# Kernel tuning notes

Hardware: AMD Instinct MI355X
Metric: run time of the kernel (lower is better)

## Reference

```python
import jax, jax.numpy as jnp
import numpy as np

D_MODEL = 1024
NUM_HEADS = 16
D_K = D_MODEL // NUM_HEADS  # 64
THETA = 10000.0


def apply_rope(x, positions, theta):
    # x: [b, h, s, d_k]; interleaved-pair RoPE
    d = x.shape[-1]
    inv_freq = theta ** (-jnp.arange(0, d, 2, dtype=jnp.float32) / d)  # [d/2]
    angles = positions.astype(jnp.float32)[:, None] * inv_freq[None, :]  # [s, d/2]
    cos = jnp.cos(angles)
    sin = jnp.sin(angles)
    x1 = x[..., 0::2]
    x2 = x[..., 1::2]
    out_even = x1 * cos - x2 * sin
    out_odd = x1 * sin + x2 * cos
    return jnp.stack([out_even, out_odd], axis=-1).reshape(x.shape)


def setup_inputs() -> dict:
    key = jax.random.key(0)
    kx, kq, kk, kv, ko = jax.random.split(key, 5)
    scale = 1.0 / np.sqrt(D_MODEL)
    return {
        "x": jax.random.normal(kx, (1, 4096, D_MODEL), dtype=jnp.float32),
        "Wq": jax.random.normal(kq, (D_MODEL, D_MODEL), dtype=jnp.float32) * scale,
        "Wk": jax.random.normal(kk, (D_MODEL, D_MODEL), dtype=jnp.float32) * scale,
        "Wv": jax.random.normal(kv, (D_MODEL, D_MODEL), dtype=jnp.float32) * scale,
        "Wo": jax.random.normal(ko, (D_MODEL, D_MODEL), dtype=jnp.float32) * scale,
    }


def reference(x, Wq, Wk, Wv, Wo):
    b, s, _ = x.shape
    # Linear (no bias, weight stored as [out, in]): y = x @ W^T
    q = jnp.einsum("bsd,ed->bse", x, Wq).reshape(b, s, NUM_HEADS, D_K).transpose(0, 2, 1, 3)
    k = jnp.einsum("bsd,ed->bse", x, Wk).reshape(b, s, NUM_HEADS, D_K).transpose(0, 2, 1, 3)
    v = jnp.einsum("bsd,ed->bse", x, Wv).reshape(b, s, NUM_HEADS, D_K).transpose(0, 2, 1, 3)

    positions = jnp.arange(s)
    q = apply_rope(q, positions, THETA)
    k = apply_rope(k, positions, THETA)

    scores = jnp.einsum("bhqd,bhkd->bhqk", q, k) / jnp.sqrt(jnp.float32(D_K))
    causal = jnp.tril(jnp.ones((s, s), dtype=bool))
    scores = jnp.where(causal, scores, -jnp.inf)
    probs = jax.nn.softmax(scores, axis=-1)
    ctx = jnp.einsum("bhqk,bhkd->bhqd", probs, v)  # [b,h,s,d_k]
    ctx = ctx.transpose(0, 2, 1, 3).reshape(b, s, D_MODEL)
    return jnp.einsum("bse,de->bsd", ctx, Wo)
```

## Files before the change

### kernel.cpp

```cpp
#include <hip/hip_runtime.h>
#include <hip/hip_bf16.h>
#include <math.h>


#define S_LEN 4096
#define DMODEL 1024
#define NHEAD 16
#define QSCALE 0.1803368801111244f

typedef __attribute__((ext_vector_type(8))) short short8;
typedef __attribute__((ext_vector_type(4))) short short4_t;
typedef __attribute__((ext_vector_type(4))) float floatx4;

static __device__ __forceinline__ void load_lds16(const void* g, void* l) {
    __builtin_amdgcn_global_load_lds((const __attribute__((address_space(1))) void*)g,
                                     (__attribute__((address_space(3))) void*)l, 16, 0, 0);
}

__global__ void cvt_all_kernel(const float* __restrict__ x,  const float* __restrict__ wq,
                               const float* __restrict__ wk, const float* __restrict__ wv,
                               const float* __restrict__ wo,
                               __hip_bfloat16* __restrict__ xb,  __hip_bfloat16* __restrict__ wqb,
                               __hip_bfloat16* __restrict__ wkb, __hip_bfloat16* __restrict__ wvb,
                               __hip_bfloat16* __restrict__ wob)
{
    const size_t NX = (size_t)S_LEN * DMODEL;
    const size_t NW = (size_t)DMODEL * DMODEL;
    size_t t = ((size_t)blockIdx.x * blockDim.x + threadIdx.x) * 4;
    const float* src; __hip_bfloat16* dst; size_t off;
    if (t < NX) { src = x; dst = xb; off = t; }
    else {
        size_t j = t - NX; int seg = (int)(j >> 20); off = j & (NW - 1);
        src = (seg == 0) ? wq : (seg == 1) ? wk : (seg == 2) ? wv : wo;
        dst = (seg == 0) ? wqb : (seg == 1) ? wkb : (seg == 2) ? wvb : wob;
    }
    float4 v = *(const float4*)(src + off);
    dst[off + 0] = __float2bfloat16(v.x);
    dst[off + 1] = __float2bfloat16(v.y);
    dst[off + 2] = __float2bfloat16(v.z);
    dst[off + 3] = __float2bfloat16(v.w);
}

__global__ __launch_bounds__(256) void qkv_gemm(
    const __hip_bfloat16* __restrict__ A,
    const __hip_bfloat16* __restrict__ Bq,
    const __hip_bfloat16* __restrict__ Bk,
    const __hip_bfloat16* __restrict__ Bv,
    __hip_bfloat16* __restrict__ Qb,
    __hip_bfloat16* __restrict__ Kb,
    __hip_bfloat16* __restrict__ Vtb)
{
    __shared__ __hip_bfloat16 As[128 * 32];
    __shared__ __hip_bfloat16 Bs[128 * 32];
    const int tid  = threadIdx.x;
    const int wave = tid >> 6;
    const int lane = tid & 63;
    const int quad = lane >> 4;
    const int l15  = lane & 15;
    const int sec  = blockIdx.x >> 3;
    const __hip_bfloat16* B = (sec == 0) ? Bq : (sec == 1) ? Bk : Bv;
    const int n0 = (blockIdx.x & 7) * 128;
    const int m0 = blockIdx.y * 128;
    const int wm = (wave & 1) * 64;
    const int wn = (wave >> 1) * 64;

    floatx4 acc[4][4] = {};

    for (int kt = 0; kt < DMODEL; kt += 32) {
        #pragma unroll
        for (int p = 0; p < 2; ++p) {
            int base = (p * 4 + wave) * 1024;
            int b    = base + lane * 16;
            int row  = b >> 6;
            int ke   = (b & 63) >> 1;
            load_lds16(A + (size_t)(m0 + row) * DMODEL + kt + ke, (char*)As + base);
            load_lds16(B + (size_t)(n0 + row) * DMODEL + kt + ke, (char*)Bs + base);
        }
        __syncthreads();
        short8 af[4], bf[4];
        #pragma unroll
        for (int i = 0; i < 4; ++i)
            af[i] = *(const short8*)(As + (wm + i * 16 + l15) * 32 + quad * 8);
        #pragma unroll
        for (int j = 0; j < 4; ++j)
            bf[j] = *(const short8*)(Bs + (wn + j * 16 + l15) * 32 + quad * 8);
        #pragma unroll
        for (int i = 0; i < 4; ++i)
            #pragma unroll
            for (int j = 0; j < 4; ++j)
                acc[i][j] = __builtin_amdgcn_mfma_f32_16x16x32_bf16(af[i], bf[j], acc[i][j], 0, 0, 0);
        __syncthreads();
    }

    float ifreq[4];
    #pragma unroll
    for (int j = 0; j < 4; ++j) {
        int d = (j * 16 + l15) & 63;
        ifreq[j] = expf(-(float)(d & ~1) * (9.210340371976184f / 64.0f));
    }
    const float scale = (sec == 0) ? QSCALE : 1.0f;
    __hip_bfloat16* dst = (sec == 0) ? Qb : Kb;
    #pragma unroll
    for (int i = 0; i < 4; ++i) {
        int rowb = m0 + wm + i * 16 + quad * 4;
        #pragma unroll
        for (int j = 0; j < 4; ++j) {
            int col = n0 + wn + j * 16 + l15;
            if (sec == 2) {
                union { short4_t v; __hip_bfloat16 b[4]; } pk;
                #pragma unroll
                for (int r = 0; r < 4; ++r) pk.b[r] = __float2bfloat16(acc[i][j][r]);
                int sw = (rowb & ~63) | ((((rowb >> 3) ^ col) & 7) << 3) | (rowb & 7);
                *(short4_t*)(Vtb + (size_t)col * S_LEN + sw) = pk.v;
            } else {
                #pragma unroll
                for (int r = 0; r < 4; ++r) {
                    int rr  = rowb + r;
                    float v = acc[i][j][r];
                    float ang = (float)rr * ifreq[j];
                    float sn, cs;
                    __sincosf(ang, &sn, &cs);
                    float pv  = __shfl_xor(v, 1);
                    float out = ((lane & 1) ? (pv * sn + v * cs)
                                            : (v * cs - pv * sn)) * scale;
                    int pc = (sec == 1) ? ((col & ~63) | ((((col >> 3) ^ rr) & 7) << 3) | (col & 7))
                                        : col;
                    dst[(size_t)rr * DMODEL + pc] = __float2bfloat16(out);
                }
            }
        }
    }
}

__global__ __launch_bounds__(256) void attn_kernel(
    const __hip_bfloat16* __restrict__ Q,
    const __hip_bfloat16* __restrict__ Kb,
    const __hip_bfloat16* __restrict__ Vt,
    __hip_bfloat16* __restrict__ CTX)
{
    __shared__ __hip_bfloat16 Ks[64 * 64];
    __shared__ __hip_bfloat16 Vs[64 * 64];
    __shared__ __hip_bfloat16 Ps[4][16 * 68];
    const int b  = blockIdx.x;
    const int h  = b & 15;
    const int g  = b >> 4;
    const int gq = g >> 4, d4 = g & 15;
    const int qt = (gq == 0) ? 63 - d4 : (gq == 1) ? 32 + d4 : (gq == 2) ? 31 - d4 : d4;
    const int s0 = qt * 64;
    const int tid  = threadIdx.x;
    const int wave = tid >> 6, lane = tid & 63;
    const int quad = lane >> 4, l15 = lane & 15;
    const int k7   = l15 & 7;
    const int W    = s0 + wave * 16;

    short8 aq[2];
    {
        const __hip_bfloat16* qp = Q + (size_t)(W + l15) * DMODEL + h * 64 + quad * 8;
        aq[0] = *(const short8*)qp;
        aq[1] = *(const short8*)(qp + 32);
    }
    floatx4 o[4] = {};
    float lp[4] = {};

    for (int kt = 0; kt <= qt; ++kt) {
        #pragma unroll
        for (int p = 0; p < 4; ++p) {
            int id   = p * 4 + wave;
            int cb   = (id & 7) * 1024;
            int bb   = cb + lane * 16;
            int row  = bb >> 7;
            int ce   = (bb & 127) >> 1;
            if (id < 8)
                load_lds16(Kb + (size_t)(kt * 64 + row) * DMODEL + h * 64 + ce, (char*)Ks + cb);
            else
                load_lds16(Vt + (size_t)(h * 64 + row) * S_LEN + kt * 64 + ce,  (char*)Vs + cb);
        }
        __syncthreads();

        const int kv0 = kt * 64;
        floatx4 sc[4];
        #pragma unroll
        for (int ni = 0; ni < 4; ++ni) {
            short8 bk0 = *(const short8*)(Ks + (ni * 16 + l15) * 64 + ((quad ^ k7) << 3));
            short8 bk1 = *(const short8*)(Ks + (ni * 16 + l15) * 64 + (((4 + quad) ^ k7) << 3));
            floatx4 s = {};
            s = __builtin_amdgcn_mfma_f32_16x16x32_bf16(aq[0], bk0, s, 0, 0, 0);
            sc[ni] = __builtin_amdgcn_mfma_f32_16x16x32_bf16(aq[1], bk1, s, 0, 0, 0);
        }

        const bool edge  = (kt == qt);
        const int  rbase = W + quad * 4;
        #pragma unroll
        for (int ni = 0; ni < 4; ++ni) {
            int col = kv0 + ni * 16 + l15;
            #pragma unroll
            for (int r = 0; r < 4; ++r) {
                float p = __builtin_amdgcn_exp2f(sc[ni][r]);
                if (edge && col > rbase + r) p = 0.0f;
                lp[r] += p;
                Ps[wave][(quad * 4 + r) * 68 + ni * 16 + l15] = __float2bfloat16(p);
            }
        }

        short8 ap[2];
        #pragma unroll
        for (int dc = 0; dc < 2; ++dc) {
            const __hip_bfloat16* pp = &Ps[wave][l15 * 68 + dc * 32 + quad * 8];
            short4_t p0 = *(const short4_t*)pp;
            short4_t p1 = *(const short4_t*)(pp + 4);
            short8 a;
            a[0] = p0[0]; a[1] = p0[1]; a[2] = p0[2]; a[3] = p0[3];
            a[4] = p1[0]; a[5] = p1[1]; a[6] = p1[2]; a[7] = p1[3];
            ap[dc] = a;
        }

        #pragma unroll
        for (int od = 0; od < 4; ++od) {
            short8 bv0 = *(const short8*)(Vs + (od * 16 + l15) * 64 + ((quad ^ k7) << 3));
            short8 bv1 = *(const short8*)(Vs + (od * 16 + l15) * 64 + (((4 + quad) ^ k7) << 3));
            o[od] = __builtin_amdgcn_mfma_f32_16x16x32_bf16(ap[0], bv0, o[od], 0, 0, 0);
            o[od] = __builtin_amdgcn_mfma_f32_16x16x32_bf16(ap[1], bv1, o[od], 0, 0, 0);
        }
        __syncthreads();
    }

    #pragma unroll
    for (int r = 0; r < 4; ++r) {
        float v = lp[r];
        v += __shfl_xor(v, 1);
        v += __shfl_xor(v, 2);
        v += __shfl_xor(v, 4);
        v += __shfl_xor(v, 8);
        lp[r] = __frcp_rn(v);
    }
    #pragma unroll
    for (int od = 0; od < 4; ++od)
        #pragma unroll
        for (int r = 0; r < 4; ++r)
            CTX[(size_t)(W + quad * 4 + r) * DMODEL + h * 64 + od * 16 + l15] =
                __float2bfloat16(o[od][r] * lp[r]);
}

__global__ __launch_bounds__(256) void out_gemm(
    const __hip_bfloat16* __restrict__ A,
    const __hip_bfloat16* __restrict__ B,
    float* __restrict__ C)
{
    __shared__ __hip_bfloat16 As[128 * 32];
    __shared__ __hip_bfloat16 Bs[64 * 32];
    const int tid  = threadIdx.x;
    const int wave = tid >> 6;
    const int lane = tid & 63;
    const int quad = lane >> 4;
    const int l15  = lane & 15;
    const int n0 = blockIdx.x * 64;
    const int m0 = blockIdx.y * 128;
    const int wm = (wave & 1) * 64;
    const int wn = (wave >> 1) * 32;

    floatx4 acc[4][2] = {};

    for (int kt = 0; kt < DMODEL; kt += 32) {
        #pragma unroll
        for (int p = 0; p < 3; ++p) {
            int id  = p * 4 + wave;
            if (id < 8) {
                int base = id * 1024;
                int b    = base + lane * 16;
                int row  = b >> 6;
                int ke   = (b & 63) >> 1;
                load_lds16(A + (size_t)(m0 + row) * DMODEL + kt + ke, (char*)As + base);
            } else {
                int base = (id - 8) * 1024;
                int b    = base + lane * 16;
                int row  = b >> 6;
                int ke   = (b & 63) >> 1;
                load_lds16(B + (size_t)(n0 + row) * DMODEL + kt + ke, (char*)Bs + base);
            }
        }
        __syncthreads();
        short8 af[4], bf[2];
        #pragma unroll
        for (int i = 0; i < 4; ++i)
            af[i] = *(const short8*)(As + (wm + i * 16 + l15) * 32 + quad * 8);
        #pragma unroll
        for (int j = 0; j < 2; ++j)
            bf[j] = *(const short8*)(Bs + (wn + j * 16 + l15) * 32 + quad * 8);
        #pragma unroll
        for (int i = 0; i < 4; ++i)
            #pragma unroll
            for (int j = 0; j < 2; ++j)
                acc[i][j] = __builtin_amdgcn_mfma_f32_16x16x32_bf16(af[i], bf[j], acc[i][j], 0, 0, 0);
        __syncthreads();
    }

    #pragma unroll
    for (int i = 0; i < 4; ++i) {
        int rowb = m0 + wm + i * 16 + quad * 4;
        #pragma unroll
        for (int j = 0; j < 2; ++j) {
            int col = n0 + wn + j * 16 + l15;
            #pragma unroll
            for (int r = 0; r < 4; ++r)
                C[(size_t)(rowb + r) * DMODEL + col] = acc[i][j][r];
        }
    }
}

extern "C" void kernel_launch(void* const* d_in, const int* in_sizes, int n_in,
                              void* d_out, int out_size, void* d_ws, size_t ws_size,
                              hipStream_t stream)
{
    const float* x  = (const float*)d_in[0];
    const float* Wq = (const float*)d_in[1];
    const float* Wk = (const float*)d_in[2];
    const float* Wv = (const float*)d_in[3];
    const float* Wo = (const float*)d_in[4];

    char* ws = (char*)d_ws;
    const size_t MB = 1024 * 1024;
    __hip_bfloat16* xb  = (__hip_bfloat16*)(ws);
    __hip_bfloat16* wqb = (__hip_bfloat16*)(ws +  8 * MB);
    __hip_bfloat16* wkb = (__hip_bfloat16*)(ws + 10 * MB);
    __hip_bfloat16* wvb = (__hip_bfloat16*)(ws + 12 * MB);
    __hip_bfloat16* wob = (__hip_bfloat16*)(ws + 14 * MB);
    __hip_bfloat16* Qb  = (__hip_bfloat16*)(ws + 16 * MB);
    __hip_bfloat16* Kbf = (__hip_bfloat16*)(ws + 24 * MB);
    __hip_bfloat16* Vtb = (__hip_bfloat16*)(ws + 32 * MB);
    __hip_bfloat16* Cx  = (__hip_bfloat16*)(ws + 40 * MB);

    cvt_all_kernel<<<8192, 256, 0, stream>>>(x, Wq, Wk, Wv, Wo, xb, wqb, wkb, wvb, wob);

    qkv_gemm<<<dim3(24, 32), 256, 0, stream>>>(xb, wqb, wkb, wvb, Qb, Kbf, Vtb);

    attn_kernel<<<1024, 256, 0, stream>>>(Qb, Kbf, Vtb, Cx);

    out_gemm<<<dim3(16, 32), 256, 0, stream>>>(Cx, wob, (float*)d_out);
}
```

Baseline: 215.8 us.

## Split KV tiles across waves with fragment-packed Q/K/V layout and direct global loads

The QKV projection now writes Q, K and V in a per-head, MFMA-fragment-ordered layout. This lets the attention kernel load operand fragments straight from global memory into registers instead of staging K/V through LDS. Each wave now handles all 64 query rows of the block and a strided subset of KV tiles (split-K across waves), and the partial outputs and row sums are combined through LDS at the end. This removes per-tile __syncthreads and LDS staging. In exchange, register pressure rises with 64 accumulators per lane, and the partial outputs are rounded to bf16 before the reduction. Since no running max is kept, the exponentials are not rescaled and rely on the prescaled scores staying small.

```diff
diff --git a/kernel.cpp b/kernel.cpp
--- a/kernel.cpp
+++ b/kernel.cpp
@@ -106,13 +106,17 @@
         #pragma unroll
         for (int j = 0; j < 4; ++j) {
             int col = n0 + wn + j * 16 + l15;
+            int h   = col >> 6;
+            int hd  = col & 63;
             if (sec == 2) {
                 union { short4_t v; __hip_bfloat16 b[4]; } pk;
                 #pragma unroll
                 for (int r = 0; r < 4; ++r) pk.b[r] = __float2bfloat16(acc[i][j][r]);
-                int sw = (rowb & ~63) | ((((rowb >> 3) ^ col) & 7) << 3) | (rowb & 7);
-                *(short4_t*)(Vtb + (size_t)col * S_LEN + sw) = pk.v;
+                int od = hd >> 4, lv = hd & 15;
+                *(short4_t*)(Vtb + (size_t)h * 262144 +
+                             (((od * 512 + (rowb >> 3)) * 16 + lv) << 3) + (rowb & 7)) = pk.v;
             } else {
+                int g = hd >> 3, jj = hd & 7;
                 #pragma unroll
                 for (int r = 0; r < 4; ++r) {
                     int rr  = rowb + r;
@@ -123,89 +127,63 @@
                     float pv  = __shfl_xor(v, 1);
                     float out = ((lane & 1) ? (pv * sn + v * cs)
                                             : (v * cs - pv * sn)) * scale;
-                    int pc = (sec == 1) ? ((col & ~63) | ((((col >> 3) ^ rr) & 7) << 3) | (col & 7))
-                                        : col;
-                    dst[(size_t)rr * DMODEL + pc] = __float2bfloat16(out);
+                    dst[(size_t)h * 262144 +
+                        ((((rr >> 4) * 8 + g) * 16 + (rr & 15)) << 3) + jj] = __float2bfloat16(out);
                 }
             }
         }
     }
 }
 
-__global__ __launch_bounds__(256) void attn_kernel(
-    const __hip_bfloat16* __restrict__ Q,
-    const __hip_bfloat16* __restrict__ Kb,
-    const __hip_bfloat16* __restrict__ Vt,
-    __hip_bfloat16* __restrict__ CTX)
-{
-    __shared__ __hip_bfloat16 Ks[64 * 64];
-    __shared__ __hip_bfloat16 Vs[64 * 64];
-    __shared__ __hip_bfloat16 Ps[4][16 * 68];
-    const int b  = blockIdx.x;
-    const int h  = b & 15;
-    const int g  = b >> 4;
-    const int gq = g >> 4, d4 = g & 15;
-    const int qt = (gq == 0) ? 63 - d4 : (gq == 1) ? 32 + d4 : (gq == 2) ? 31 - d4 : d4;
-    const int s0 = qt * 64;
-    const int tid  = threadIdx.x;
-    const int wave = tid >> 6, lane = tid & 63;
-    const int quad = lane >> 4, l15 = lane & 15;
-    const int k7   = l15 & 7;
-    const int W    = s0 + wave * 16;
-
-    short8 aq[2];
-    {
-        const __hip_bfloat16* qp = Q + (size_t)(W + l15) * DMODEL + h * 64 + quad * 8;
-        aq[0] = *(const short8*)qp;
-        aq[1] = *(const short8*)(qp + 32);
-    }
-    floatx4 o[4] = {};
-    float lp[4] = {};
-
-    for (int kt = 0; kt <= qt; ++kt) {
-        #pragma unroll
-        for (int p = 0; p < 4; ++p) {
-            int id   = p * 4 + wave;
-            int cb   = (id & 7) * 1024;
-            int bb   = cb + lane * 16;
-            int row  = bb >> 7;
-            int ce   = (bb & 127) >> 1;
-            if (id < 8)
-                load_lds16(Kb + (size_t)(kt * 64 + row) * DMODEL + h * 64 + ce, (char*)Ks + cb);
-            else
-                load_lds16(Vt + (size_t)(h * 64 + row) * S_LEN + kt * 64 + ce,  (char*)Vs + cb);
-        }
-        __syncthreads();
-
-        const int kv0 = kt * 64;
-        floatx4 sc[4];
+template<bool EDGE>
+static __device__ __forceinline__ void attn_tile(
+    int kt, int quad, int l15,
+    const __hip_bfloat16* __restrict__ Kh, const __hip_bfloat16* __restrict__ Vh,
+    const short8 aq[4][2], floatx4 o[4][4], float lp[4][4],
+    __hip_bfloat16* __restrict__ PsW)
+{
+    asm volatile("s_waitcnt lgkmcnt(0)" ::: "memory");
+
+    short8 kf[4][2], vf[4][2];
+    #pragma unroll
+    for (int ni = 0; ni < 4; ++ni)
+        #pragma unroll
+        for (int dc = 0; dc < 2; ++dc)
+            kf[ni][dc] = *(const short8*)(Kh + (size_t)(((((kt*4 + ni)*8 + dc*4 + quad)*16 + l15) << 3)));
+    #pragma unroll
+    for (int od = 0; od < 4; ++od)
+        #pragma unroll
+        for (int dc = 0; dc < 2; ++dc)
+            vf[od][dc] = *(const short8*)(Vh + (size_t)((((od*512 + kt*8 + dc*4 + quad)*16 + l15) << 3)));
+
+    #pragma unroll
+    for (int g = 0; g < 4; ++g) {
+        floatx4 st[4];
         #pragma unroll
         for (int ni = 0; ni < 4; ++ni) {
-            short8 bk0 = *(const short8*)(Ks + (ni * 16 + l15) * 64 + ((quad ^ k7) << 3));
-            short8 bk1 = *(const short8*)(Ks + (ni * 16 + l15) * 64 + (((4 + quad) ^ k7) << 3));
-            floatx4 s = {};
-            s = __builtin_amdgcn_mfma_f32_16x16x32_bf16(aq[0], bk0, s, 0, 0, 0);
-            sc[ni] = __builtin_amdgcn_mfma_f32_16x16x32_bf16(aq[1], bk1, s, 0, 0, 0);
-        }
-
-        const bool edge  = (kt == qt);
-        const int  rbase = W + quad * 4;
+            floatx4 z = {};
+            floatx4 s = __builtin_amdgcn_mfma_f32_16x16x32_bf16(aq[g][0], kf[ni][0], z, 0, 0, 0);
+            st[ni]    = __builtin_amdgcn_mfma_f32_16x16x32_bf16(aq[g][1], kf[ni][1], s, 0, 0, 0);
+        }
         #pragma unroll
         for (int ni = 0; ni < 4; ++ni) {
-            int col = kv0 + ni * 16 + l15;
             #pragma unroll
             for (int r = 0; r < 4; ++r) {
-                float p = __builtin_amdgcn_exp2f(sc[ni][r]);
-                if (edge && col > rbase + r) p = 0.0f;
-                lp[r] += p;
-                Ps[wave][(quad * 4 + r) * 68 + ni * 16 + l15] = __float2bfloat16(p);
+                float e = __builtin_amdgcn_exp2f(st[ni][r]);
+                if (EDGE) {
+                    if (ni * 16 + l15 > g * 16 + quad * 4 + r) e = 0.0f;
+                }
+                lp[g][r] += e;
+                PsW[(g * 16 + quad * 4 + r) * 68 + ni * 16 + l15] = __float2bfloat16(e);
             }
         }
-
+    }
+    #pragma unroll
+    for (int g = 0; g < 4; ++g) {
         short8 ap[2];
         #pragma unroll
         for (int dc = 0; dc < 2; ++dc) {
-            const __hip_bfloat16* pp = &Ps[wave][l15 * 68 + dc * 32 + quad * 8];
+            const __hip_bfloat16* pp = PsW + (g * 16 + l15) * 68 + dc * 32 + quad * 8;
             short4_t p0 = *(const short4_t*)pp;
             short4_t p1 = *(const short4_t*)(pp + 4);
             short8 a;
@@ -213,32 +191,93 @@
             a[4] = p1[0]; a[5] = p1[1]; a[6] = p1[2]; a[7] = p1[3];
             ap[dc] = a;
         }
-
         #pragma unroll
         for (int od = 0; od < 4; ++od) {
-            short8 bv0 = *(const short8*)(Vs + (od * 16 + l15) * 64 + ((quad ^ k7) << 3));
-            short8 bv1 = *(const short8*)(Vs + (od * 16 + l15) * 64 + (((4 + quad) ^ k7) << 3));
-            o[od] = __builtin_amdgcn_mfma_f32_16x16x32_bf16(ap[0], bv0, o[od], 0, 0, 0);
-            o[od] = __builtin_amdgcn_mfma_f32_16x16x32_bf16(ap[1], bv1, o[od], 0, 0, 0);
-        }
-        __syncthreads();
-    }
+            o[g][od] = __builtin_amdgcn_mfma_f32_16x16x32_bf16(ap[0], vf[od][0], o[g][od], 0, 0, 0);
+            o[g][od] = __builtin_amdgcn_mfma_f32_16x16x32_bf16(ap[1], vf[od][1], o[g][od], 0, 0, 0);
+        }
+    }
+}
+
+__global__ __launch_bounds__(256) void attn_kernel(
+    const __hip_bfloat16* __restrict__ Q,
+    const __hip_bfloat16* __restrict__ Kp,
+    const __hip_bfloat16* __restrict__ Vp,
+    __hip_bfloat16* __restrict__ CTX)
+{
+    __shared__ __hip_bfloat16 Buf[4][64 * 68];
+    __shared__ float LPw[4][64];
+    const int b  = blockIdx.x;
+    const int h  = b & 15;
+    const int u  = 63 - (b >> 4);
+    const int tid  = threadIdx.x;
+    const int wave = tid >> 6, lane = tid & 63;
+    const int quad = lane >> 4, l15 = lane & 15;
+
+    const __hip_bfloat16* Qh = Q  + (size_t)h * 262144;
+    const __hip_bfloat16* Kh = Kp + (size_t)h * 262144;
+    const __hip_bfloat16* Vh = Vp + (size_t)h * 262144;
+    __hip_bfloat16* PsW = &Buf[wave][0];
+
+    short8 aq[4][2];
+    #pragma unroll
+    for (int g = 0; g < 4; ++g)
+        #pragma unroll
+        for (int dc = 0; dc < 2; ++dc)
+            aq[g][dc] = *(const short8*)(Qh + (size_t)(((((u*4 + g)*8 + dc*4 + quad)*16 + l15) << 3)));
+
+    floatx4 o[4][4] = {};
+    float lp[4][4] = {};
+
+    for (int kt = wave; kt < u; kt += 4)
+        attn_tile<false>(kt, quad, l15, Kh, Vh, aq, o, lp, PsW);
+    if ((u & 3) == wave)
+        attn_tile<true>(u, quad, l15, Kh, Vh, aq, o, lp, PsW);
+
+    #pragma unroll
+    for (int g = 0; g < 4; ++g)
+        #pragma unroll
+        for (int r = 0; r < 4; ++r) {
+            float v = lp[g][r];
+            v += __shfl_xor(v, 1);
+            v += __shfl_xor(v, 2);
+            v += __shfl_xor(v, 4);
+            v += __shfl_xor(v, 8);
+            lp[g][r] = v;
+        }
+    asm volatile("s_waitcnt lgkmcnt(0)" ::: "memory");
+    if (l15 == 0) {
+        #pragma unroll
+        for (int g = 0; g < 4; ++g)
+            #pragma unroll
+            for (int r = 0; r < 4; ++r)
+                LPw[wave][g * 16 + quad * 4 + r] = lp[g][r];
+    }
+    #pragma unroll
+    for (int g = 0; g < 4; ++g)
+        #pragma unroll
+        for (int od = 0; od < 4; ++od)
+            #pragma unroll
+            for (int r = 0; r < 4; ++r)
+                Buf[wave][(g * 16 + quad * 4 + r) * 68 + od * 16 + l15] =
+                    __float2bfloat16(o[g][od][r]);
+    __syncthreads();
 
     #pragma unroll
     for (int r = 0; r < 4; ++r) {
-        float v = lp[r];
-        v += __shfl_xor(v, 1);
-        v += __shfl_xor(v, 2);
-        v += __shfl_xor(v, 4);
-        v += __shfl_xor(v, 8);
-        lp[r] = __frcp_rn(v);
-    }
-    #pragma unroll
-    for (int od = 0; od < 4; ++od)
-        #pragma unroll
-        for (int r = 0; r < 4; ++r)
-            CTX[(size_t)(W + quad * 4 + r) * DMODEL + h * 64 + od * 16 + l15] =
-                __float2bfloat16(o[od][r] * lp[r]);
+        int q = wave * 16 + quad * 4 + r;
+        float ls = LPw[0][q] + LPw[1][q] + LPw[2][q] + LPw[3][q];
+        float rl = __frcp_rn(ls);
+        #pragma unroll
+        for (int od = 0; od < 4; ++od) {
+            float s = 0.0f;
+            #pragma unroll
+            for (int sl = 0; sl < 4; ++sl)
+                s += __bfloat162float(Buf[sl][q * 68 + od * 16 + l15]);
+            CTX[(size_t)(u * 64 + q) * DMODEL + h * 64 + od * 16 + l15] =
+                __float2bfloat16(s * rl);
+        }
+    }
 }
 
 __global__ __launch_bounds__(256) void out_gemm(
```

After: 221.5 us. +2.7%, slower.
